# Performance work log

Measured on AMD Instinct MI355X. Metric: run time of the kernel, lower is better.

The kernel has to match this reference:

```python
import jax, jax.numpy as jnp
import numpy as np


def _conv1x1(x, w, b):
    # x: [B, Cin, H, W]; w: [Cout, Cin, 1, 1]; b: [Cout]
    y = jnp.einsum('bchw,oc->bohw', x, w[:, :, 0, 0])
    return y + b[None, :, None, None]


def setup_inputs() -> dict:
    key = jax.random.key(0)
    ks = jax.random.split(key, 9)
    B, C, H, W = 8, 256, 64, 64
    Cq = C // 4
    sc = 0.05
    return {
        'x': jax.random.normal(ks[0], (B, C, H, W), jnp.float32),
        'query_weight': jax.random.normal(ks[1], (Cq, C, 1, 1), jnp.float32) * sc,
        'query_bias': jax.random.normal(ks[2], (Cq,), jnp.float32) * sc,
        'key_weight': jax.random.normal(ks[3], (Cq, C, 1, 1), jnp.float32) * sc,
        'key_bias': jax.random.normal(ks[4], (Cq,), jnp.float32) * sc,
        'value_weight': jax.random.normal(ks[5], (C, C, 1, 1), jnp.float32) * sc,
        'value_bias': jax.random.normal(ks[6], (C,), jnp.float32) * sc,
        'gamma_weight': jax.random.normal(ks[7], (C, C, 1, 1), jnp.float32) * sc,
        'gamma_bias': jax.random.normal(ks[8], (C,), jnp.float32) * sc,
    }


def reference(x, query_weight, query_bias, key_weight, key_bias,
              value_weight, value_bias, gamma_weight, gamma_bias):
    B, C, H, W = x.shape
    N = H * W
    q = _conv1x1(x, query_weight, query_bias).reshape(B, -1, N)   # [B, Cq, N]
    k = _conv1x1(x, key_weight, key_bias).reshape(B, -1, N)       # [B, Cq, N]
    v = _conv1x1(x, value_weight, value_bias).reshape(B, C, N)    # [B, C, N]
    # energy[b, i, j] = sum_c q[b, c, i] * k[b, c, j]
    energy = jnp.einsum('bci,bcj->bij', q, k)                     # [B, N, N]
    energy = jax.nn.elu(energy) / N
    out = jnp.einsum('bcn,bnm->bcm', v, energy).reshape(B, C, H, W)
    return _conv1x1(out, gamma_weight, gamma_bias)
```

## Files before the change

kernel.cpp:

```cpp
#include <hip/hip_runtime.h>
#include <cmath>

#define BB 8
#define CC 256
#define CQ 64
#define NN 4096
constexpr float INV_N = 1.0f / 4096.0f;

typedef __attribute__((ext_vector_type(8))) short short8;
typedef __attribute__((ext_vector_type(4))) short short4v;
typedef __attribute__((ext_vector_type(4))) float float4v;

__device__ __forceinline__ short f2bf(float f) {
  union { float f; unsigned u; } x; x.f = f;
  unsigned r = x.u + 0x7fffu + ((x.u >> 16) & 1u);
  return (short)(r >> 16);
}

__global__ void wconv_kernel(const float* __restrict__ wq,
                             const float* __restrict__ wk,
                             const float* __restrict__ wv,
                             const float* __restrict__ wg,
                             short* __restrict__ wqb, short* __restrict__ wkb,
                             short* __restrict__ wvb, short* __restrict__ wgb) {
  const int t = blockIdx.x * 256 + threadIdx.x;
  const float* src;
  short* dst;
  int idx;
  if (t < 4096)        { src = wq; dst = wqb; idx = t; }
  else if (t < 8192)   { src = wk; dst = wkb; idx = t - 4096; }
  else if (t < 24576)  { src = wv; dst = wvb; idx = t - 8192; }
  else                 { src = wg; dst = wgb; idx = t - 24576; }
  const float4 v = *reinterpret_cast<const float4*>(&src[(size_t)idx * 4]);
  short4v o;
  o[0] = f2bf(v.x); o[1] = f2bf(v.y); o[2] = f2bf(v.z); o[3] = f2bf(v.w);
  *reinterpret_cast<short4v*>(&dst[(size_t)idx * 4]) = o;
}

__global__ __launch_bounds__(256, 2) void qkv_kernel(
    const float* __restrict__ X,
    const short* __restrict__ wqb, const float* __restrict__ bq,
    const short* __restrict__ wkb, const float* __restrict__ bk,
    const short* __restrict__ wvb, const float* __restrict__ bv,
    short* __restrict__ qt, short* __restrict__ kt, short* __restrict__ vbf) {
  __shared__ short xt[64 * 264];
  const int tid = threadIdx.x;
  const int wid = tid >> 6;
  const int lane = tid & 63, quad = lane >> 4, l16 = lane & 15;
  const int b = blockIdx.x, n0 = blockIdx.y * 64;

  float4 xb[16];
#pragma unroll
  for (int p = 0; p < 16; ++p) {
    const int idx = p * 256 + tid;
    const int c = idx >> 4;
    const int n4 = (idx & 15) * 4;
    xb[p] = *reinterpret_cast<const float4*>(
        &X[((size_t)b * CC + c) * NN + n0 + n4]);
  }
#pragma unroll
  for (int p = 0; p < 16; ++p) {
    const int idx = p * 256 + tid;
    const int c = idx >> 4;
    const int n4 = (idx & 15) * 4;
    xt[(n4 + 0) * 264 + c] = f2bf(xb[p].x);
    xt[(n4 + 1) * 264 + c] = f2bf(xb[p].y);
    xt[(n4 + 2) * 264 + c] = f2bf(xb[p].z);
    xt[(n4 + 3) * 264 + c] = f2bf(xb[p].w);
  }
  __syncthreads();

  short8 bfr[8][4];
#pragma unroll
  for (int kk = 0; kk < 8; ++kk)
#pragma unroll
    for (int tm = 0; tm < 4; ++tm)
      bfr[kk][tm] = *reinterpret_cast<const short8*>(
          &xt[(tm * 16 + l16) * 264 + kk * 32 + quad * 8]);
  __syncthreads();

  short* Os0 = xt;
  short* Os1 = xt + 4608;

  for (int ch = 0; ch < 6; ++ch) {
    const short* W; const float* bias; int obase;
    if (ch == 0)      { W = wqb; bias = bq; obase = 0; }
    else if (ch == 1) { W = wkb; bias = bk; obase = 0; }
    else { W = wvb + (size_t)(ch - 2) * 64 * CC; bias = bv + (ch - 2) * 64; obase = (ch - 2) * 64; }

    const short* wrow = &W[(size_t)(wid * 16 + l16) * CC + quad * 8];
    short8 wf[8];
#pragma unroll
    for (int kk = 0; kk < 8; ++kk)
      wf[kk] = *reinterpret_cast<const short8*>(wrow + kk * 32);

    float4v acc[4];
#pragma unroll
    for (int tm = 0; tm < 4; ++tm) acc[tm] = float4v{0.f, 0.f, 0.f, 0.f};
#pragma unroll
    for (int kk = 0; kk < 8; ++kk)
#pragma unroll
      for (int tm = 0; tm < 4; ++tm)
        acc[tm] = __builtin_amdgcn_mfma_f32_16x16x32_bf16(wf[kk], bfr[kk][tm], acc[tm], 0, 0, 0);

    if (ch < 2) {
      short* dst = (ch == 0) ? qt : kt;
#pragma unroll
      for (int tm = 0; tm < 4; ++tm) {
        short4v pk;
#pragma unroll
        for (int r = 0; r < 4; ++r)
          pk[r] = f2bf(acc[tm][r] + bias[wid * 16 + quad * 4 + r]);
        *reinterpret_cast<short4v*>(
            &dst[((size_t)b * NN + n0 + tm * 16 + l16) * 64 + wid * 16 + quad * 4]) = pk;
      }
    } else {
      short* Os = (ch & 1) ? Os1 : Os0;
#pragma unroll
      for (int tm = 0; tm < 4; ++tm)
#pragma unroll
        for (int r = 0; r < 4; ++r)
          Os[(wid * 16 + quad * 4 + r) * 72 + tm * 16 + l16] =
              f2bf(acc[tm][r] + bias[wid * 16 + quad * 4 + r]);
      __syncthreads();
      const int o = tid >> 2, ng = (tid & 3) * 16;
      const short8 s0 = *reinterpret_cast<const short8*>(&Os[o * 72 + ng]);
      const short8 s1 = *reinterpret_cast<const short8*>(&Os[o * 72 + ng + 8]);
      short* vp = &vbf[((size_t)b * CC + obase + o) * NN + n0 + ng];
      *reinterpret_cast<short8*>(vp) = s0;
      *reinterpret_cast<short8*>(vp + 8) = s1;
    }
  }
}

__global__ __launch_bounds__(256, 2) void attn_kernel(
    const short* __restrict__ qt, const short* __restrict__ kt,
    const short* __restrict__ vbf, const short* __restrict__ wgb,
    const float* __restrict__ bg, float* __restrict__ out) {
  __shared__ short smem[16896];
  short* Es0 = smem;
  short* Es1 = smem + 4608;
  short* Outs = smem;

  const int tid = threadIdx.x;
  const int wid = tid >> 6;
  const int lane = tid & 63, quad = lane >> 4, l16 = lane & 15;
  const int b = blockIdx.x, m0 = blockIdx.y * 64;

  short8 bkf[4][2];
#pragma unroll
  for (int tm = 0; tm < 4; ++tm)
#pragma unroll
    for (int kk = 0; kk < 2; ++kk)
      bkf[tm][kk] = *reinterpret_cast<const short8*>(
          &kt[((size_t)b * NN + m0 + tm * 16 + l16) * 64 + kk * 32 + quad * 8]);

  const short* qp = &qt[((size_t)b * NN + wid * 16 + l16) * 64 + quad * 8];
  const short* vrow[4];
#pragma unroll
  for (int tc = 0; tc < 4; ++tc)
    vrow[tc] = &vbf[((size_t)b * CC + wid * 64 + tc * 16 + l16) * NN + quad * 8];

  float4v acc[4][4];
#pragma unroll
  for (int i = 0; i < 4; ++i)
#pragma unroll
    for (int j = 0; j < 4; ++j) acc[i][j] = float4v{0.f, 0.f, 0.f, 0.f};

  short8 avA[4][2], avB[4][2];
#pragma unroll
  for (int tc = 0; tc < 4; ++tc) {
    avA[tc][0] = *reinterpret_cast<const short8*>(vrow[tc]);
    avA[tc][1] = *reinterpret_cast<const short8*>(vrow[tc] + 32);
  }
  short8 aqA0 = *reinterpret_cast<const short8*>(qp + (size_t)1 * 4096);
  short8 aqA1 = *reinterpret_cast<const short8*>(qp + (size_t)1 * 4096 + 32);
  short8 aqB0, aqB1;
  {
    const short8 aq0 = *reinterpret_cast<const short8*>(qp);
    const short8 aq1 = *reinterpret_cast<const short8*>(qp + 32);
#pragma unroll
    for (int tm = 0; tm < 4; ++tm) {
      float4v t = {0.f, 0.f, 0.f, 0.f};
      t = __builtin_amdgcn_mfma_f32_16x16x32_bf16(aq0, bkf[tm][0], t, 0, 0, 0);
      t = __builtin_amdgcn_mfma_f32_16x16x32_bf16(aq1, bkf[tm][1], t, 0, 0, 0);
      short4v pk;
#pragma unroll
      for (int r = 0; r < 4; ++r) {
        float sv = t[r];
        sv = (sv > 0.f) ? sv : (__expf(sv) - 1.f);
        pk[r] = f2bf(sv);
      }
      *reinterpret_cast<short4v*>(
          &Es0[(tm * 16 + l16) * 72 + wid * 16 + quad * 4]) = pk;
    }
  }
  __syncthreads();

  auto seg = [&](int it, short8 (&avc)[4][2], short8 (&avn)[4][2],
                 short8& aqc0, short8& aqc1, short8& aqn0, short8& aqn1) {
    const int nb1 = (it + 1) * 64;
#pragma unroll
    for (int tc = 0; tc < 4; ++tc) {
      avn[tc][0] = *reinterpret_cast<const short8*>(vrow[tc] + nb1);
      avn[tc][1] = *reinterpret_cast<const short8*>(vrow[tc] + nb1 + 32);
    }
    aqn0 = *reinterpret_cast<const short8*>(qp + (size_t)(it + 2) * 4096);
    aqn1 = *reinterpret_cast<const short8*>(qp + (size_t)(it + 2) * 4096 + 32);

    short* Esr = (it & 1) ? Es1 : Es0;
    short* Esw = (it & 1) ? Es0 : Es1;

    float4v s[4];
    if (it < 63) {
#pragma unroll
      for (int tm = 0; tm < 4; ++tm) {
        float4v t = {0.f, 0.f, 0.f, 0.f};
        t = __builtin_amdgcn_mfma_f32_16x16x32_bf16(aqc0, bkf[tm][0], t, 0, 0, 0);
        t = __builtin_amdgcn_mfma_f32_16x16x32_bf16(aqc1, bkf[tm][1], t, 0, 0, 0);
        s[tm] = t;
      }
    }

#pragma unroll
    for (int tm = 0; tm < 4; ++tm) {
      const short8 be0 = *reinterpret_cast<const short8*>(
          &Esr[(tm * 16 + l16) * 72 + quad * 8]);
      const short8 be1 = *reinterpret_cast<const short8*>(
          &Esr[(tm * 16 + l16) * 72 + 32 + quad * 8]);
#pragma unroll
      for (int tc = 0; tc < 4; ++tc) {
        acc[tc][tm] = __builtin_amdgcn_mfma_f32_16x16x32_bf16(avc[tc][0], be0, acc[tc][tm], 0, 0, 0);
        acc[tc][tm] = __builtin_amdgcn_mfma_f32_16x16x32_bf16(avc[tc][1], be1, acc[tc][tm], 0, 0, 0);
      }
    }

    if (it < 63) {
#pragma unroll
      for (int tm = 0; tm < 4; ++tm) {
        short4v pk;
#pragma unroll
        for (int r = 0; r < 4; ++r) {
          float sv = s[tm][r];
          sv = (sv > 0.f) ? sv : (__expf(sv) - 1.f);
          pk[r] = f2bf(sv);
        }
        *reinterpret_cast<short4v*>(
            &Esw[(tm * 16 + l16) * 72 + wid * 16 + quad * 4]) = pk;
      }
    }
    __syncthreads();
  };

  for (int it = 0; it < 64; it += 2) {
    seg(it,     avA, avB, aqA0, aqA1, aqB0, aqB1);
    seg(it + 1, avB, avA, aqB0, aqB1, aqA0, aqA1);
  }

#pragma unroll
  for (int tc = 0; tc < 4; ++tc)
#pragma unroll
    for (int tm = 0; tm < 4; ++tm) {
      short4v pk;
#pragma unroll
      for (int r = 0; r < 4; ++r) pk[r] = f2bf(acc[tc][tm][r] * INV_N);
      *reinterpret_cast<short4v*>(
          &Outs[(tm * 16 + l16) * 264 + wid * 64 + tc * 16 + quad * 4]) = pk;
    }
  __syncthreads();

#pragma unroll
  for (int i = 0; i < 4; ++i)
#pragma unroll
    for (int j = 0; j < 4; ++j) acc[i][j] = float4v{0.f, 0.f, 0.f, 0.f};

  for (int ks8 = 0; ks8 < 8; ++ks8) {
    short8 ag[4];
#pragma unroll
    for (int to = 0; to < 4; ++to)
      ag[to] = *reinterpret_cast<const short8*>(
          &wgb[(size_t)(wid * 64 + to * 16 + l16) * CC + ks8 * 32 + quad * 8]);
    short8 bo[4];
#pragma unroll
    for (int tm = 0; tm < 4; ++tm)
      bo[tm] = *reinterpret_cast<const short8*>(
          &Outs[(tm * 16 + l16) * 264 + ks8 * 32 + quad * 8]);
#pragma unroll
    for (int to = 0; to < 4; ++to)
#pragma unroll
      for (int tm = 0; tm < 4; ++tm)
        acc[to][tm] =
            __builtin_amdgcn_mfma_f32_16x16x32_bf16(ag[to], bo[tm], acc[to][tm], 0, 0, 0);
  }

#pragma unroll
  for (int to = 0; to < 4; ++to) {
#pragma unroll
    for (int r = 0; r < 4; ++r) {
      const int o = wid * 64 + to * 16 + quad * 4 + r;
      const float bgv = bg[o];
#pragma unroll
      for (int tm = 0; tm < 4; ++tm) {
        out[((size_t)b * CC + o) * NN + m0 + tm * 16 + l16] =
            acc[to][tm][r] + bgv;
      }
    }
  }
}

extern "C" void kernel_launch(void* const* d_in, const int* in_sizes, int n_in,
                              void* d_out, int out_size, void* d_ws,
                              size_t ws_size, hipStream_t stream) {
  const float* x  = (const float*)d_in[0];
  const float* wq = (const float*)d_in[1];
  const float* bq = (const float*)d_in[2];
  const float* wk = (const float*)d_in[3];
  const float* bk = (const float*)d_in[4];
  const float* wv = (const float*)d_in[5];
  const float* bv = (const float*)d_in[6];
  const float* wg = (const float*)d_in[7];
  const float* bg = (const float*)d_in[8];
  float* out = (float*)d_out;

  short* qt  = (short*)d_ws;
  short* kt  = qt + (size_t)BB * NN * CQ;
  short* vbf = kt + (size_t)BB * NN * CQ;
  short* wqb = vbf + (size_t)BB * CC * NN;
  short* wkb = wqb + (size_t)CQ * CC;
  short* wvb = wkb + (size_t)CQ * CC;
  short* wgb = wvb + (size_t)CC * CC;

  wconv_kernel<<<dim3(160), 256, 0, stream>>>(wq, wk, wv, wg, wqb, wkb, wvb, wgb);
  qkv_kernel<<<dim3(BB, NN / 64), 256, 0, stream>>>(x, wqb, bq, wkb, bk, wvb, bv,
                                                    qt, kt, vbf);
  attn_kernel<<<dim3(BB, NN / 64), 256, 0, stream>>>(qt, kt, vbf, wgb, bg, out);
}
```

Baseline: 272.3 us.

## Widen attention tile to 128 output columns with 512-thread blocks

The attention kernel now handles 128 output positions per block with 8 waves instead of 64 with 4. Each wave covers 32 value channels across all 128 columns, so each V tile is read once per 128 columns instead of once per 64, halving V traffic. It also drops the register double-buffering of V/Q loads in favour of plain per-iteration loads, adds s_setprio around the MFMA section, and splits the gamma projection into two 64-column halves. The cost is half as many blocks (256), more registers per thread at 512 threads, and less latency hiding for the global loads.

```diff
diff --git a/kernel.cpp b/kernel.cpp
--- a/kernel.cpp
+++ b/kernel.cpp
@@ -133,178 +133,174 @@
   }
 }
 
-__global__ __launch_bounds__(256, 2) void attn_kernel(
+__global__ __launch_bounds__(512, 2) void attn_kernel(
     const short* __restrict__ qt, const short* __restrict__ kt,
     const short* __restrict__ vbf, const short* __restrict__ wgb,
     const float* __restrict__ bg, float* __restrict__ out) {
-  __shared__ short smem[16896];
+  __shared__ short smem[18432];
   short* Es0 = smem;
-  short* Es1 = smem + 4608;
+  short* Es1 = smem + 9216;
   short* Outs = smem;
 
   const int tid = threadIdx.x;
   const int wid = tid >> 6;
   const int lane = tid & 63, quad = lane >> 4, l16 = lane & 15;
-  const int b = blockIdx.x, m0 = blockIdx.y * 64;
-
-  short8 bkf[4][2];
-#pragma unroll
-  for (int tm = 0; tm < 4; ++tm)
-#pragma unroll
-    for (int kk = 0; kk < 2; ++kk)
-      bkf[tm][kk] = *reinterpret_cast<const short8*>(
-          &kt[((size_t)b * NN + m0 + tm * 16 + l16) * 64 + kk * 32 + quad * 8]);
-
-  const short* qp = &qt[((size_t)b * NN + wid * 16 + l16) * 64 + quad * 8];
-  const short* vrow[4];
-#pragma unroll
-  for (int tc = 0; tc < 4; ++tc)
-    vrow[tc] = &vbf[((size_t)b * CC + wid * 64 + tc * 16 + l16) * NN + quad * 8];
-
-  float4v acc[4][4];
-#pragma unroll
-  for (int i = 0; i < 4; ++i)
-#pragma unroll
-    for (int j = 0; j < 4; ++j) acc[i][j] = float4v{0.f, 0.f, 0.f, 0.f};
-
-  short8 avA[4][2], avB[4][2];
-#pragma unroll
-  for (int tc = 0; tc < 4; ++tc) {
-    avA[tc][0] = *reinterpret_cast<const short8*>(vrow[tc]);
-    avA[tc][1] = *reinterpret_cast<const short8*>(vrow[tc] + 32);
-  }
-  short8 aqA0 = *reinterpret_cast<const short8*>(qp + (size_t)1 * 4096);
-  short8 aqA1 = *reinterpret_cast<const short8*>(qp + (size_t)1 * 4096 + 32);
-  short8 aqB0, aqB1;
-  {
-    const short8 aq0 = *reinterpret_cast<const short8*>(qp);
-    const short8 aq1 = *reinterpret_cast<const short8*>(qp + 32);
-#pragma unroll
-    for (int tm = 0; tm < 4; ++tm) {
-      float4v t = {0.f, 0.f, 0.f, 0.f};
-      t = __builtin_amdgcn_mfma_f32_16x16x32_bf16(aq0, bkf[tm][0], t, 0, 0, 0);
-      t = __builtin_amdgcn_mfma_f32_16x16x32_bf16(aq1, bkf[tm][1], t, 0, 0, 0);
-      short4v pk;
-#pragma unroll
-      for (int r = 0; r < 4; ++r) {
-        float sv = t[r];
-        sv = (sv > 0.f) ? sv : (__expf(sv) - 1.f);
-        pk[r] = f2bf(sv);
-      }
-      *reinterpret_cast<short4v*>(
-          &Es0[(tm * 16 + l16) * 72 + wid * 16 + quad * 4]) = pk;
-    }
+  const int b = blockIdx.x, m0 = blockIdx.y * 128;
+
+  short8 bkf[2];
+#pragma unroll
+  for (int kk = 0; kk < 2; ++kk)
+    bkf[kk] = *reinterpret_cast<const short8*>(
+        &kt[((size_t)b * NN + m0 + wid * 16 + l16) * 64 + kk * 32 + quad * 8]);
+
+  const short* qb = &qt[((size_t)b * NN + l16) * 64 + quad * 8];
+  const short* vrow[2];
+#pragma unroll
+  for (int tc = 0; tc < 2; ++tc)
+    vrow[tc] = &vbf[((size_t)b * CC + wid * 32 + tc * 16 + l16) * NN + quad * 8];
+
+  float4v acc[2][8];
+#pragma unroll
+  for (int i = 0; i < 2; ++i)
+#pragma unroll
+    for (int j = 0; j < 8; ++j) acc[i][j] = float4v{0.f, 0.f, 0.f, 0.f};
+
+#pragma unroll
+  for (int ng = 0; ng < 4; ++ng) {
+    const short8 a0 = *reinterpret_cast<const short8*>(qb + (size_t)(ng * 16) * 64);
+    const short8 a1 = *reinterpret_cast<const short8*>(qb + (size_t)(ng * 16) * 64 + 32);
+    float4v t = {0.f, 0.f, 0.f, 0.f};
+    t = __builtin_amdgcn_mfma_f32_16x16x32_bf16(a0, bkf[0], t, 0, 0, 0);
+    t = __builtin_amdgcn_mfma_f32_16x16x32_bf16(a1, bkf[1], t, 0, 0, 0);
+    short4v pk;
+#pragma unroll
+    for (int r = 0; r < 4; ++r) {
+      float sv = t[r];
+      sv = (sv > 0.f) ? sv : (__expf(sv) - 1.f);
+      pk[r] = f2bf(sv);
+    }
+    *reinterpret_cast<short4v*>(
+        &Es0[(wid * 16 + l16) * 72 + ng * 16 + quad * 4]) = pk;
   }
   __syncthreads();
 
-  auto seg = [&](int it, short8 (&avc)[4][2], short8 (&avn)[4][2],
-                 short8& aqc0, short8& aqc1, short8& aqn0, short8& aqn1) {
-    const int nb1 = (it + 1) * 64;
-#pragma unroll
-    for (int tc = 0; tc < 4; ++tc) {
-      avn[tc][0] = *reinterpret_cast<const short8*>(vrow[tc] + nb1);
-      avn[tc][1] = *reinterpret_cast<const short8*>(vrow[tc] + nb1 + 32);
-    }
-    aqn0 = *reinterpret_cast<const short8*>(qp + (size_t)(it + 2) * 4096);
-    aqn1 = *reinterpret_cast<const short8*>(qp + (size_t)(it + 2) * 4096 + 32);
-
+  for (int it = 0; it < 64; ++it) {
     short* Esr = (it & 1) ? Es1 : Es0;
     short* Esw = (it & 1) ? Es0 : Es1;
-
+    const int nb = it * 64;
+
+    short8 av[2][2];
+#pragma unroll
+    for (int tc = 0; tc < 2; ++tc) {
+      av[tc][0] = *reinterpret_cast<const short8*>(vrow[tc] + nb);
+      av[tc][1] = *reinterpret_cast<const short8*>(vrow[tc] + nb + 32);
+    }
+    short8 aq[4][2];
+    if (it < 63) {
+#pragma unroll
+      for (int ng = 0; ng < 4; ++ng) {
+        const size_t qoff = (size_t)((it + 1) * 64 + ng * 16) * 64;
+        aq[ng][0] = *reinterpret_cast<const short8*>(qb + qoff);
+        aq[ng][1] = *reinterpret_cast<const short8*>(qb + qoff + 32);
+      }
+    }
+
+    __builtin_amdgcn_s_setprio(1);
     float4v s[4];
     if (it < 63) {
 #pragma unroll
-      for (int tm = 0; tm < 4; ++tm) {
+      for (int ng = 0; ng < 4; ++ng) {
         float4v t = {0.f, 0.f, 0.f, 0.f};
-        t = __builtin_amdgcn_mfma_f32_16x16x32_bf16(aqc0, bkf[tm][0], t, 0, 0, 0);
-        t = __builtin_amdgcn_mfma_f32_16x16x32_bf16(aqc1, bkf[tm][1], t, 0, 0, 0);
-        s[tm] = t;
-      }
-    }
-
-#pragma unroll
-    for (int tm = 0; tm < 4; ++tm) {
+        t = __builtin_amdgcn_mfma_f32_16x16x32_bf16(aq[ng][0], bkf[0], t, 0, 0, 0);
+        t = __builtin_amdgcn_mfma_f32_16x16x32_bf16(aq[ng][1], bkf[1], t, 0, 0, 0);
+        s[ng] = t;
+      }
+    }
+#pragma unroll
+    for (int tm = 0; tm < 8; ++tm) {
       const short8 be0 = *reinterpret_cast<const short8*>(
           &Esr[(tm * 16 + l16) * 72 + quad * 8]);
       const short8 be1 = *reinterpret_cast<const short8*>(
           &Esr[(tm * 16 + l16) * 72 + 32 + quad * 8]);
 #pragma unroll
-      for (int tc = 0; tc < 4; ++tc) {
-        acc[tc][tm] = __builtin_amdgcn_mfma_f32_16x16x32_bf16(avc[tc][0], be0, acc[tc][tm], 0, 0, 0);
-        acc[tc][tm] = __builtin_amdgcn_mfma_f32_16x16x32_bf16(avc[tc][1], be1, acc[tc][tm], 0, 0, 0);
-      }
-    }
+      for (int tc = 0; tc < 2; ++tc) {
+        acc[tc][tm] = __builtin_amdgcn_mfma_f32_16x16x32_bf16(av[tc][0], be0, acc[tc][tm], 0, 0, 0);
+        acc[tc][tm] = __builtin_amdgcn_mfma_f32_16x16x32_bf16(av[tc][1], be1, acc[tc][tm], 0, 0, 0);
+      }
+    }
+    __builtin_amdgcn_s_setprio(0);
 
     if (it < 63) {
 #pragma unroll
-      for (int tm = 0; tm < 4; ++tm) {
+      for (int ng = 0; ng < 4; ++ng) {
         short4v pk;
 #pragma unroll
         for (int r = 0; r < 4; ++r) {
-          float sv = s[tm][r];
+          float sv = s[ng][r];
           sv = (sv > 0.f) ? sv : (__expf(sv) - 1.f);
           pk[r] = f2bf(sv);
         }
         *reinterpret_cast<short4v*>(
-            &Esw[(tm * 16 + l16) * 72 + wid * 16 + quad * 4]) = pk;
+            &Esw[(wid * 16 + l16) * 72 + ng * 16 + quad * 4]) = pk;
       }
     }
     __syncthreads();
-  };
-
-  for (int it = 0; it < 64; it += 2) {
-    seg(it,     avA, avB, aqA0, aqA1, aqB0, aqB1);
-    seg(it + 1, avB, avA, aqB0, aqB1, aqA0, aqA1);
-  }
-
-#pragma unroll
-  for (int tc = 0; tc < 4; ++tc)
-#pragma unroll
-    for (int tm = 0; tm < 4; ++tm) {
-      short4v pk;
-#pragma unroll
-      for (int r = 0; r < 4; ++r) pk[r] = f2bf(acc[tc][tm][r] * INV_N);
-      *reinterpret_cast<short4v*>(
-          &Outs[(tm * 16 + l16) * 264 + wid * 64 + tc * 16 + quad * 4]) = pk;
-    }
-  __syncthreads();
-
-#pragma unroll
-  for (int i = 0; i < 4; ++i)
-#pragma unroll
-    for (int j = 0; j < 4; ++j) acc[i][j] = float4v{0.f, 0.f, 0.f, 0.f};
-
-  for (int ks8 = 0; ks8 < 8; ++ks8) {
-    short8 ag[4];
-#pragma unroll
-    for (int to = 0; to < 4; ++to)
-      ag[to] = *reinterpret_cast<const short8*>(
-          &wgb[(size_t)(wid * 64 + to * 16 + l16) * CC + ks8 * 32 + quad * 8]);
-    short8 bo[4];
-#pragma unroll
-    for (int tm = 0; tm < 4; ++tm)
-      bo[tm] = *reinterpret_cast<const short8*>(
-          &Outs[(tm * 16 + l16) * 264 + ks8 * 32 + quad * 8]);
-#pragma unroll
-    for (int to = 0; to < 4; ++to)
-#pragma unroll
-      for (int tm = 0; tm < 4; ++tm)
-        acc[to][tm] =
-            __builtin_amdgcn_mfma_f32_16x16x32_bf16(ag[to], bo[tm], acc[to][tm], 0, 0, 0);
-  }
-
-#pragma unroll
-  for (int to = 0; to < 4; ++to) {
-#pragma unroll
-    for (int r = 0; r < 4; ++r) {
-      const int o = wid * 64 + to * 16 + quad * 4 + r;
-      const float bgv = bg[o];
-#pragma unroll
-      for (int tm = 0; tm < 4; ++tm) {
-        out[((size_t)b * CC + o) * NN + m0 + tm * 16 + l16] =
-            acc[to][tm][r] + bgv;
-      }
-    }
+  }
+
+#pragma unroll
+  for (int mh = 0; mh < 2; ++mh) {
+#pragma unroll
+    for (int tmh = 0; tmh < 4; ++tmh)
+#pragma unroll
+      for (int tc = 0; tc < 2; ++tc) {
+        short4v pk;
+#pragma unroll
+        for (int r = 0; r < 4; ++r)
+          pk[r] = f2bf(acc[tc][mh * 4 + tmh][r] * INV_N);
+        *reinterpret_cast<short4v*>(
+            &Outs[(tmh * 16 + l16) * 264 + wid * 32 + tc * 16 + quad * 4]) = pk;
+      }
+    __syncthreads();
+
+    float4v acg[2][4];
+#pragma unroll
+    for (int i = 0; i < 2; ++i)
+#pragma unroll
+      for (int j = 0; j < 4; ++j) acg[i][j] = float4v{0.f, 0.f, 0.f, 0.f};
+
+    for (int ks8 = 0; ks8 < 8; ++ks8) {
+      short8 ag[2];
+#pragma unroll
+      for (int to = 0; to < 2; ++to)
+        ag[to] = *reinterpret_cast<const short8*>(
+            &wgb[(size_t)(wid * 32 + to * 16 + l16) * CC + ks8 * 32 + quad * 8]);
+      short8 bo[4];
+#pragma unroll
+      for (int tmh = 0; tmh < 4; ++tmh)
+        bo[tmh] = *reinterpret_cast<const short8*>(
+            &Outs[(tmh * 16 + l16) * 264 + ks8 * 32 + quad * 8]);
+#pragma unroll
+      for (int to = 0; to < 2; ++to)
+#pragma unroll
+        for (int tmh = 0; tmh < 4; ++tmh)
+          acg[to][tmh] =
+              __builtin_amdgcn_mfma_f32_16x16x32_bf16(ag[to], bo[tmh], acg[to][tmh], 0, 0, 0);
+    }
+
+#pragma unroll
+    for (int to = 0; to < 2; ++to) {
+#pragma unroll
+      for (int r = 0; r < 4; ++r) {
+        const int o = wid * 32 + to * 16 + quad * 4 + r;
+        const float bgv = bg[o];
+#pragma unroll
+        for (int tmh = 0; tmh < 4; ++tmh) {
+          out[((size_t)b * CC + o) * NN + m0 + mh * 64 + tmh * 16 + l16] =
+              acg[to][tmh][r] + bgv;
+        }
+      }
+    }
+    __syncthreads();
   }
 }
 
@@ -333,5 +329,5 @@
   wconv_kernel<<<dim3(160), 256, 0, stream>>>(wq, wk, wv, wg, wqb, wkb, wvb, wgb);
   qkv_kernel<<<dim3(BB, NN / 64), 256, 0, stream>>>(x, wqb, bq, wkb, bk, wvb, bv,
                                                     qt, kt, vbf);
-  attn_kernel<<<dim3(BB, NN / 64), 256, 0, stream>>>(qt, kt, vbf, wgb, bg, out);
-}
+  attn_kernel<<<dim3(BB, NN / 128), 512, 0, stream>>>(qt, kt, vbf, wgb, bg, out);
+}
```

After: 352.0 us. 1.29x slower.
